# Performance work log

Measured on AMD Instinct MI355X. Metric: run time of the kernel, lower is better.

## Reference

```python
import jax, jax.numpy as jnp
import numpy as np

B, N_OBJ, OBJ_D = 256, 36, 2048
ATT_D, EMB_D, DEC_D, VOCAB, T = 1024, 1024, 1024, 10000, 20


def setup_inputs() -> dict:
    key = jax.random.key(0)
    ks = jax.random.split(key, 16)
    s = lambda *d: 1.0 / np.sqrt(d[-1])
    inp = {
        'encoder_out': jax.random.normal(ks[0], (B, EMB_D), jnp.float32),
        'objects': jax.random.normal(ks[1], (B, N_OBJ, OBJ_D), jnp.float32),
        'encoded_captions': jax.random.randint(ks[2], (B, T), 0, VOCAB),
        'caption_lengths': jax.random.randint(ks[3], (B, 1), 1, T + 1),
        'emb_table': jax.random.normal(ks[4], (VOCAB, EMB_D), jnp.float32) * 0.02,
        'W_enc_att': jax.random.normal(ks[5], (ATT_D, OBJ_D), jnp.float32) * s(OBJ_D),
        'b_enc_att': jnp.zeros((ATT_D,), jnp.float32),
        'W_dec_att': jax.random.normal(ks[6], (ATT_D, DEC_D), jnp.float32) * s(DEC_D),
        'b_dec_att': jnp.zeros((ATT_D,), jnp.float32),
        'w_full_att': jax.random.normal(ks[7], (1, ATT_D), jnp.float32) * s(ATT_D),
        'b_full_att': jnp.zeros((1,), jnp.float32),
        'W_fbeta': jax.random.normal(ks[8], (OBJ_D, DEC_D), jnp.float32) * s(DEC_D),
        'b_fbeta': jnp.zeros((OBJ_D,), jnp.float32),
        'W_ih': jax.random.normal(ks[9], (4 * DEC_D, EMB_D + OBJ_D), jnp.float32) * s(EMB_D + OBJ_D),
        'W_hh': jax.random.normal(ks[10], (4 * DEC_D, DEC_D), jnp.float32) * s(DEC_D),
        'b_ih': jnp.zeros((4 * DEC_D,), jnp.float32),
        'b_hh': jnp.zeros((4 * DEC_D,), jnp.float32),
        'W_fc': jax.random.normal(ks[11], (VOCAB, DEC_D), jnp.float32) * s(DEC_D),
        'b_fc': jnp.zeros((VOCAB,), jnp.float32),
    }
    return inp


def reference(encoder_out, objects, encoded_captions, caption_lengths,
              emb_table, W_enc_att, b_enc_att, W_dec_att, b_dec_att,
              w_full_att, b_full_att, W_fbeta, b_fbeta,
              W_ih, W_hh, b_ih, b_hh, W_fc, b_fc):
    lengths = caption_lengths[:, 0]
    sort_ind = jnp.argsort(-lengths)  # descending
    lengths = lengths[sort_ind]
    encoder_out = encoder_out[sort_ind]
    objects = objects[sort_ind]
    encoded_captions = encoded_captions[sort_ind]

    embeddings = emb_table[encoded_captions]  # (B, T, E)
    # step t input: encoder_out at t=0, embeddings[:, t-1] afterwards
    step_x = jnp.concatenate([encoder_out[:, None, :], embeddings[:, : T - 1, :]], axis=1)  # (B,T,E)

    att1 = jnp.einsum('bno,ao->bna', objects, W_enc_att) + b_enc_att  # (B,N,A), h-independent

    def step(carry, xs):
        h, c = carry
        x_t, t = xs  # (B,E), scalar
        active = (t < lengths)[:, None]  # (B,1) -- batch_size_t masking (lengths sorted desc)
        att2 = h @ W_dec_att.T + b_dec_att  # (B,A)
        e = (jax.nn.relu(att1 + att2[:, None, :]) @ w_full_att[0] + b_full_att[0])  # (B,N)
        alpha = jax.nn.softmax(e, axis=1)
        awe = jnp.einsum('bn,bno->bo', alpha, objects)  # (B,O)
        gate = jax.nn.sigmoid(h @ W_fbeta.T + b_fbeta)
        awe = gate * awe
        gates = jnp.concatenate([x_t, awe], axis=-1) @ W_ih.T + b_ih + h @ W_hh.T + b_hh
        i, f, g, o = jnp.split(gates, 4, axis=-1)  # torch LSTMCell order
        c_new = jax.nn.sigmoid(f) * c + jax.nn.sigmoid(i) * jnp.tanh(g)
        h_new = jax.nn.sigmoid(o) * jnp.tanh(c_new)
        h = jnp.where(active, h_new, h)
        c = jnp.where(active, c_new, c)
        preds = h_new @ W_fc.T + b_fc  # dropout in eval mode = identity
        preds = jnp.where(active, preds, 0.0)
        alpha = jnp.where(active, alpha, 0.0)
        return (h, c), (preds, alpha)

    h0 = jnp.zeros((B, DEC_D), objects.dtype)
    c0 = jnp.zeros((B, DEC_D), objects.dtype)
    xs = (jnp.swapaxes(step_x, 0, 1), jnp.arange(T))
    _, (preds, alphas) = jax.lax.scan(step, (h0, c0), xs)
    predictions = jnp.swapaxes(preds, 0, 1)  # (B,T,V)
    alphas = jnp.swapaxes(alphas, 0, 1)      # (B,T,N)
    return predictions, encoded_captions, lengths, alphas, sort_ind
```

## Files before the change

### kernel.cpp

```cpp
#include <hip/hip_runtime.h>
#include <hip/hip_bf16.h>
#include <cstdint>
#include <cstddef>

#define BB 256
#define TT 20
#define NOBJ 36
#define OBJD 2048
#define ATTD 1024
#define DECD 1024
#define VOCAB 10000
#define NBIG  17168
#define NBIGP 17280
#define NSPLIT 7168

typedef unsigned short u16;
typedef __attribute__((ext_vector_type(8))) short short8v;
typedef __attribute__((ext_vector_type(4))) float float4v;

__device__ inline u16 f2bf(float f) {
    __hip_bfloat16 h = __float2bfloat16(f);
    return *reinterpret_cast<u16*>(&h);
}
__device__ inline float bu(u16 u) {
    union { unsigned int i; float f; } x;
    x.i = ((unsigned int)u) << 16;
    return x.f;
}
__device__ inline float sigf(float x) { return 1.f / (1.f + expf(-x)); }

__device__ inline void gload16(const u16* g, u16* l) {
    __builtin_amdgcn_global_load_lds(
        (const __attribute__((address_space(1))) unsigned int*)g,
        (__attribute__((address_space(3))) unsigned int*)l, 16, 0, 0);
}

__global__ __launch_bounds__(256) void sort_kernel(
    const int* __restrict__ lens, int* __restrict__ sidx, int* __restrict__ slen,
    int* __restrict__ cnt, float* __restrict__ out_len, float* __restrict__ out_sind)
{
    __shared__ int L[BB];
    __shared__ int SL[BB];
    const int i = threadIdx.x;
    const int li = lens[i];
    L[i] = li;
    __syncthreads();
    int r = 0;
    for (int j = 0; j < BB; ++j) {
        const int lj = L[j];
        if (lj > li || (lj == li && j < i)) r++;
    }
    sidx[r] = i;
    slen[r] = li;
    SL[r] = li;
    out_sind[r] = (float)i;
    out_len[r]  = (float)li;
    __syncthreads();
    if (i < TT) {
        int cc = 0;
        for (int b = 0; b < BB; ++b) cc += (SL[b] > i);
        cnt[i] = cc;
    }
}

__global__ __launch_bounds__(256) void meta_kernel(
    const int* __restrict__ caps, const int* __restrict__ sidx,
    float* __restrict__ out_caps)
{
    const int idx = blockIdx.x * 256 + threadIdx.x;
    const int p = idx / TT, t = idx % TT;
    out_caps[idx] = (float)caps[sidx[p] * TT + t];
}

__global__ __launch_bounds__(256) void gather_objs(
    const float* __restrict__ objs, const int* __restrict__ sidx,
    u16* __restrict__ objsb)
{
    const int row = blockIdx.x;
    const int b = row / NOBJ, n = row - b * NOBJ;
    const float* src = objs + ((size_t)sidx[b] * NOBJ + n) * OBJD;
    u16* dst = objsb + (size_t)row * OBJD;
    const int tid = threadIdx.x;
    #pragma unroll
    for (int j = 0; j < 2; ++j) {
        float4 v = ((const float4*)src)[tid + 256 * j];
        ushort4 s;
        s.x = f2bf(v.x); s.y = f2bf(v.y); s.z = f2bf(v.z); s.w = f2bf(v.w);
        ((ushort4*)dst)[tid + 256 * j] = s;
    }
}

__global__ __launch_bounds__(256) void convWbig(
    const float* __restrict__ Wda, const float* __restrict__ bda,
    const float* __restrict__ Wfb, const float* __restrict__ bfb,
    const float* __restrict__ Whh,
    const float* __restrict__ Wfc, const float* __restrict__ bfc,
    u16* __restrict__ Wb, float* __restrict__ bcat)
{
    const int n = blockIdx.x;
    const int tid = threadIdx.x;
    const float* src = nullptr;
    float bb = 0.f;
    if (n < 1024)        { src = Wda + (size_t)n * 1024;            bb = bda[n]; }
    else if (n < 3072)   { src = Wfb + (size_t)(n - 1024) * 1024;   bb = bfb[n - 1024]; }
    else if (n < 7168)   { src = Whh + (size_t)(n - 3072) * 1024;   bb = 0.f; }
    else if (n < NBIG)   { src = Wfc + (size_t)(n - 7168) * 1024;   bb = bfc[n - 7168]; }
    u16* dst = Wb + (size_t)n * 1024;
    ushort4 s;
    if (src) {
        float4 v = ((const float4*)src)[tid];
        s.x = f2bf(v.x); s.y = f2bf(v.y); s.z = f2bf(v.z); s.w = f2bf(v.w);
    } else { s.x = s.y = s.z = s.w = 0; }
    ((ushort4*)dst)[tid] = s;
    if (tid == 0) bcat[n] = bb;
}

__global__ __launch_bounds__(256) void convWih(
    const float* __restrict__ Wih, const float* __restrict__ bih,
    const float* __restrict__ bhh, u16* __restrict__ Wb, float* __restrict__ bsum)
{
    const int n = blockIdx.x;
    const int tid = threadIdx.x;
    const float* src = Wih + (size_t)n * 3072;
    u16* dst = Wb + (size_t)n * 3072;
    #pragma unroll
    for (int j = 0; j < 3; ++j) {
        float4 v = ((const float4*)src)[tid + 256 * j];
        ushort4 s;
        s.x = f2bf(v.x); s.y = f2bf(v.y); s.z = f2bf(v.z); s.w = f2bf(v.w);
        ((ushort4*)dst)[tid + 256 * j] = s;
    }
    if (tid == 0) bsum[n] = bih[n] + bhh[n];
}

__global__ __launch_bounds__(256) void convWea(
    const float* __restrict__ Wea, u16* __restrict__ Wb)
{
    const int n = blockIdx.x;
    const int tid = threadIdx.x;
    const float* src = Wea + (size_t)n * OBJD;
    u16* dst = Wb + (size_t)n * OBJD;
    #pragma unroll
    for (int j = 0; j < 2; ++j) {
        float4 v = ((const float4*)src)[tid + 256 * j];
        ushort4 s;
        s.x = f2bf(v.x); s.y = f2bf(v.y); s.z = f2bf(v.z); s.w = f2bf(v.w);
        ((ushort4*)dst)[tid + 256 * j] = s;
    }
}

__global__ __launch_bounds__(256) void embed_kernel(
    const float* __restrict__ enc, const int* __restrict__ caps,
    const float* __restrict__ emb, const int* __restrict__ sidx,
    u16* __restrict__ Xb)
{
    const int blk = blockIdx.x;
    const int t = blk >> 8;
    const int b = blk & 255;
    const int sb = sidx[b];
    const float* src = (t == 0) ? (enc + (size_t)sb * DECD)
                                : (emb + (size_t)caps[sb * TT + (t - 1)] * DECD);
    const int tid = threadIdx.x;
    float4 v = ((const float4*)src)[tid];
    ushort4 s;
    s.x = f2bf(v.x); s.y = f2bf(v.y); s.z = f2bf(v.z); s.w = f2bf(v.w);
    ((ushort4*)(Xb + (size_t)blk * DECD))[tid] = s;
}

__global__ __launch_bounds__(256) void zero_hc(float* __restrict__ h, float* __restrict__ c)
{
    const int idx = blockIdx.x * 256 + threadIdx.x;
    if (idx < BB * DECD) h[idx] = 0.f;
    else                 c[idx - BB * DECD] = 0.f;
}

__global__ __launch_bounds__(256) void hcat0_kernel(
    const float* __restrict__ bcat, float* __restrict__ Hcat)
{
    const int col4 = blockIdx.x * 256 + threadIdx.x;
    const int m = blockIdx.y;
    ((float4*)(Hcat + (size_t)m * 7168))[col4] = ((const float4*)bcat)[col4];
}

__global__ __launch_bounds__(256) void gemm128(
    const u16* __restrict__ A, int lda,
    const u16* __restrict__ B, int ldb,
    const float* __restrict__ bias,
    float* __restrict__ Cf, u16* __restrict__ Cb, int ldc,
    int Nreal, int kzlen, size_t zCstride, int pairM,
    int nsplit, float* __restrict__ C2, int ldc2, const int* __restrict__ cntp)
{
    __shared__ u16 As[3][128 * 32];
    __shared__ u16 Bs[3][128 * 32];
    const int tid = threadIdx.x;
    const int lane = tid & 63;
    const int w = tid >> 6;
    const int wr = w >> 1, wc = w & 1;
    int nIdx, mIdx;
    if (pairM) { nIdx = blockIdx.x >> 1; mIdx = blockIdx.x & 1; }
    else       { nIdx = blockIdx.x;      mIdx = blockIdx.y; }
    const int m0 = mIdx * 128;
    const int n0 = nIdx * 128;
    const int kbase = blockIdx.z * kzlen;
    A += kbase;
    B += kbase;
    if (Cf) Cf += (size_t)blockIdx.z * zCstride;

    const int act = cntp ? *cntp : (1 << 30);
    float4v acc[4][4];
    #pragma unroll
    for (int i = 0; i < 4; ++i)
        #pragma unroll
        for (int j = 0; j < 4; ++j) acc[i][j] = (float4v){0.f, 0.f, 0.f, 0.f};

    if (m0 < act) {
        const int r0 = (w * 2 + 0) * 16 + (lane >> 2);
        const int r1 = (w * 2 + 1) * 16 + (lane >> 2);
        const int s0 = (lane & 3) ^ ((r0 >> 1) & 3);
        const int s1 = (lane & 3) ^ ((r1 >> 1) & 3);
        const u16* gA0 = A + (size_t)(m0 + r0) * lda + s0 * 8;
        const u16* gA1 = A + (size_t)(m0 + r1) * lda + s1 * 8;
        const u16* gB0 = B + (size_t)(n0 + r0) * ldb + s0 * 8;
        const u16* gB1 = B + (size_t)(n0 + r1) * ldb + s1 * 8;
        const int la0 = (w * 2 + 0) * 16 * 32;
        const int la1 = (w * 2 + 1) * 16 * 32;

        int ia[4], ib[4];
        #pragma unroll
        for (int mi = 0; mi < 4; ++mi) {
            const int r = wr * 64 + mi * 16 + (lane & 15);
            ia[mi] = r * 32 + (((lane >> 4) ^ ((r >> 1) & 3)) << 3);
        }
        #pragma unroll
        for (int nj = 0; nj < 4; ++nj) {
            const int r = wc * 64 + nj * 16 + (lane & 15);
            ib[nj] = r * 32 + (((lane >> 4) ^ ((r >> 1) & 3)) << 3);
        }

        const int nk = kzlen >> 5;
        #pragma unroll
        for (int p = 0; p < 3; ++p) {
            if (p < nk) {
                const int ko = p * 32;
                gload16(gA0 + ko, &As[p][la0]);
                gload16(gA1 + ko, &As[p][la1]);
                gload16(gB0 + ko, &Bs[p][la0]);
                gload16(gB1 + ko, &Bs[p][la1]);
            }
        }
        int cur = 0;
        for (int it = 0; it < nk; ++it) {
            const int rem = nk - 1 - it;
            if (rem >= 2)      asm volatile("s_waitcnt vmcnt(8)" ::: "memory");
            else if (rem == 1) asm volatile("s_waitcnt vmcnt(4)" ::: "memory");
            else               asm volatile("s_waitcnt vmcnt(0)" ::: "memory");
            __builtin_amdgcn_s_barrier();
            short8v av[4], bv[4];
            #pragma unroll
            for (int mi = 0; mi < 4; ++mi) av[mi] = *(const short8v*)&As[cur][ia[mi]];
            #pragma unroll
            for (int nj = 0; nj < 4; ++nj) bv[nj] = *(const short8v*)&Bs[cur][ib[nj]];
            __builtin_amdgcn_s_setprio(1);
            #pragma unroll
            for (int mi = 0; mi < 4; ++mi)
                #pragma unroll
                for (int nj = 0; nj < 4; ++nj)
                    acc[mi][nj] = __builtin_amdgcn_mfma_f32_16x16x32_bf16(
                        av[mi], bv[nj], acc[mi][nj], 0, 0, 0);
            __builtin_amdgcn_s_setprio(0);
            __builtin_amdgcn_s_barrier();
            if (it + 3 < nk) {
                const int ko = (it + 3) * 32;
                gload16(gA0 + ko, &As[cur][la0]);
                gload16(gA1 + ko, &As[cur][la1]);
                gload16(gB0 + ko, &Bs[cur][la0]);
                gload16(gB1 + ko, &Bs[cur][la1]);
            }
            cur = (cur == 2) ? 0 : cur + 1;
        }
    }

    #pragma unroll
    for (int mi = 0; mi < 4; ++mi) {
        const int mbase = m0 + wr * 64 + mi * 16 + ((lane >> 4) << 2);
        #pragma unroll
        for (int nj = 0; nj < 4; ++nj) {
            const int n = n0 + wc * 64 + nj * 16 + (lane & 15);
            if (n >= Nreal) continue;
            const float bval = bias ? bias[n] : 0.f;
            #pragma unroll
            for (int r = 0; r < 4; ++r) {
                const int m = mbase + r;
                const float v = acc[mi][nj][r] + bval;
                if (n < nsplit) {
                    if (Cb) Cb[(size_t)m * ldc + n] = f2bf(v);
                    else    Cf[(size_t)m * ldc + n] = v;
                } else {
                    C2[(size_t)m * ldc2 + (n - nsplit)] = (m < act) ? v : 0.f;
                }
            }
        }
    }
}

__global__ __launch_bounds__(256) void attn_kernel(
    const u16* __restrict__ att1b, const float* __restrict__ Hcat,
    const u16* __restrict__ objsb,
    const float* __restrict__ wfa, const float* __restrict__ bfa,
    const int* __restrict__ slen, int t,
    float* __restrict__ out_alph, u16* __restrict__ aweb)
{
    const int b = blockIdx.x, z = blockIdx.y, tid = threadIdx.x;
    const bool active = t < slen[b];
    if (!active) {
        if (z == 0 && tid < NOBJ)
            out_alph[((size_t)b * TT + t) * NOBJ + tid] = 0.f;
        return;
    }
    __shared__ float wred[4][40];
    __shared__ float es[40];
    __shared__ float alph[40];
    const int lane = tid & 63, w = tid >> 6;
    const float* hrow = Hcat + (size_t)b * 7168;
    const float4 h4 = ((const float4*)hrow)[tid];
    const float4 w4 = ((const float4*)wfa)[tid];
    const u16* a1base = att1b + (size_t)b * NOBJ * ATTD;

    float ep[NOBJ];
    #pragma unroll
    for (int n = 0; n < NOBJ; ++n) {
        ushort4 a4 = ((const ushort4*)(a1base + (size_t)n * ATTD))[tid];
        const float v0 = fmaxf(bu(a4.x) + h4.x, 0.f);
        const float v1 = fmaxf(bu(a4.y) + h4.y, 0.f);
        const float v2 = fmaxf(bu(a4.z) + h4.z, 0.f);
        const float v3 = fmaxf(bu(a4.w) + h4.w, 0.f);
        ep[n] = v0 * w4.x + v1 * w4.y + v2 * w4.z + v3 * w4.w;
    }
    #pragma unroll
    for (int n = 0; n < NOBJ; ++n) {
        float p = ep[n];
        #pragma unroll
        for (int off = 32; off > 0; off >>= 1) p += __shfl_down(p, off, 64);
        if (lane == 0) wred[w][n] = p;
    }
    __syncthreads();
    if (tid < NOBJ)
        es[tid] = wred[0][tid] + wred[1][tid] + wred[2][tid] + wred[3][tid] + bfa[0];
    __syncthreads();
    if (tid < 64) {
        float mv = (tid < NOBJ) ? es[tid] : -1e30f;
        #pragma unroll
        for (int off = 32; off > 0; off >>= 1) mv = fmaxf(mv, __shfl_xor(mv, off, 64));
        float e = (tid < NOBJ) ? expf(es[tid] - mv) : 0.f;
        float s = e;
        #pragma unroll
        for (int off = 32; off > 0; off >>= 1) s += __shfl_xor(s, off, 64);
        if (tid < NOBJ) alph[tid] = e / s;
    }
    __syncthreads();
    if (z == 0 && tid < NOBJ)
        out_alph[((size_t)b * TT + t) * NOBJ + tid] = alph[tid];

    float acc[4] = {0.f, 0.f, 0.f, 0.f};
    const u16* ob = objsb + (size_t)b * NOBJ * OBJD + z * 1024 + tid * 4;
    #pragma unroll 4
    for (int n = 0; n < NOBJ; ++n) {
        const ushort4 ov = *(const ushort4*)(ob + (size_t)n * OBJD);
        const float al = alph[n];
        acc[0] = fmaf(al, bu(ov.x), acc[0]);
        acc[1] = fmaf(al, bu(ov.y), acc[1]);
        acc[2] = fmaf(al, bu(ov.z), acc[2]);
        acc[3] = fmaf(al, bu(ov.w), acc[3]);
    }
    const float4 g0 = *(const float4*)(hrow + 1024 + z * 1024 + tid * 4);
    ushort4 st;
    st.x = f2bf(acc[0] * sigf(g0.x));
    st.y = f2bf(acc[1] * sigf(g0.y));
    st.z = f2bf(acc[2] * sigf(g0.z));
    st.w = f2bf(acc[3] * sigf(g0.w));
    *(ushort4*)&aweb[(size_t)b * 2048 + z * 1024 + tid * 4] = st;
}

__global__ __launch_bounds__(256) void lstm_kernel(
    const float* __restrict__ G2p, const u16* __restrict__ Gxb,
    const float* __restrict__ Hcat,
    float* __restrict__ h, float* __restrict__ c, u16* __restrict__ hb,
    const int* __restrict__ slen, int t)
{
    const int idx = blockIdx.x * 256 + threadIdx.x;
    const int b = idx >> 8, d4 = idx & 255;
    if (t >= slen[b]) return;
    const float4* pw = (const float4*)(Hcat + (size_t)b * 7168 + 3072);
    const u16* gx = Gxb + ((size_t)(t * BB + b)) * 4096;

    float4 g[4];
    #pragma unroll
    for (int q = 0; q < 4; ++q) {
        const ushort4 xv = ((const ushort4*)(gx + q * 1024))[d4];
        float4 s;
        s.x = bu(xv.x); s.y = bu(xv.y); s.z = bu(xv.z); s.w = bu(xv.w);
        const float4 hv = pw[q * 256 + d4];
        s.x += hv.x; s.y += hv.y; s.z += hv.z; s.w += hv.w;
        #pragma unroll
        for (int p = 0; p < 4; ++p) {
            const float4 pv = ((const float4*)G2p)[(size_t)p * (BB * 1024) + b * 1024 + q * 256 + d4];
            s.x += pv.x; s.y += pv.y; s.z += pv.z; s.w += pv.w;
        }
        g[q] = s;
    }
    float4* hp = (float4*)(h + (size_t)b * 1024);
    float4* cp = (float4*)(c + (size_t)b * 1024);
    const float4 cold = cp[d4];
    float4 cn, hn;
    {
        const float si = sigf(g[0].x), sf = sigf(g[1].x), so = sigf(g[3].x);
        cn.x = sf * cold.x + si * tanhf(g[2].x); hn.x = so * tanhf(cn.x);
    }
    {
        const float si = sigf(g[0].y), sf = sigf(g[1].y), so = sigf(g[3].y);
        cn.y = sf * cold.y + si * tanhf(g[2].y); hn.y = so * tanhf(cn.y);
    }
    {
        const float si = sigf(g[0].z), sf = sigf(g[1].z), so = sigf(g[3].z);
        cn.z = sf * cold.z + si * tanhf(g[2].z); hn.z = so * tanhf(cn.z);
    }
    {
        const float si = sigf(g[0].w), sf = sigf(g[1].w), so = sigf(g[3].w);
        cn.w = sf * cold.w + si * tanhf(g[2].w); hn.w = so * tanhf(cn.w);
    }
    hp[d4] = hn;
    cp[d4] = cn;
    ushort4 s;
    s.x = f2bf(hn.x); s.y = f2bf(hn.y); s.z = f2bf(hn.z); s.w = f2bf(hn.w);
    ((ushort4*)(hb + (size_t)b * 1024))[d4] = s;
}

extern "C" void kernel_launch(void* const* d_in, const int* in_sizes, int n_in,
                              void* d_out, int out_size, void* d_ws, size_t ws_size,
                              hipStream_t stream)
{
    const float* enc  = (const float*)d_in[0];
    const float* objs = (const float*)d_in[1];
    const int*   caps = (const int*)d_in[2];
    const int*   clen = (const int*)d_in[3];
    const float* emb  = (const float*)d_in[4];
    const float* Wea  = (const float*)d_in[5];
    const float* bea  = (const float*)d_in[6];
    const float* Wda  = (const float*)d_in[7];
    const float* bda  = (const float*)d_in[8];
    const float* wfa  = (const float*)d_in[9];
    const float* bfa  = (const float*)d_in[10];
    const float* Wfb  = (const float*)d_in[11];
    const float* bfb  = (const float*)d_in[12];
    const float* Wih  = (const float*)d_in[13];
    const float* Whh  = (const float*)d_in[14];
    const float* bih  = (const float*)d_in[15];
    const float* bhh  = (const float*)d_in[16];
    const float* Wfc  = (const float*)d_in[17];
    const float* bfc  = (const float*)d_in[18];

    float* outP     = (float*)d_out;
    float* out_caps = outP + (size_t)BB * TT * VOCAB;
    float* out_len  = out_caps + BB * TT;
    float* out_alph = out_len + BB;
    float* out_sind = out_alph + (size_t)BB * TT * NOBJ;

    char* wp = (char*)d_ws;
    auto alloc = [&](size_t bytes) -> void* {
        void* r = (void*)wp;
        wp += (bytes + 255) & ~(size_t)255;
        return r;
    };
    int*   sidx  = (int*)alloc(BB * 4);
    int*   slen  = (int*)alloc(BB * 4);
    int*   cnt   = (int*)alloc(32 * 4);
    u16*   objsb = (u16*)alloc((size_t)BB * NOBJ * OBJD * 2);
    u16*   Wbigb = (u16*)alloc((size_t)NBIGP * 1024 * 2);
    float* bcat  = (float*)alloc(NBIGP * 4);
    u16*   Wihb  = (u16*)alloc((size_t)4096 * 3072 * 2);
    float* bsum  = (float*)alloc(4096 * 4);
    u16*   Weab  = (u16*)alloc((size_t)1024 * OBJD * 2);
    u16*   att1b = (u16*)alloc((size_t)BB * NOBJ * ATTD * 2);
    u16*   Xb    = (u16*)alloc((size_t)TT * BB * DECD * 2);
    u16*   Gxb   = (u16*)alloc((size_t)TT * BB * 4096 * 2);
    float* Hcat  = (float*)alloc((size_t)BB * 7168 * 4);
    u16*   aweb  = (u16*)alloc((size_t)BB * 2048 * 2);
    float* G2p   = (float*)alloc((size_t)4 * BB * 4096 * 4);
    float* h     = (float*)alloc((size_t)BB * DECD * 4);
    float* c     = (float*)alloc((size_t)BB * DECD * 4);
    u16*   hb    = (u16*)alloc((size_t)BB * DECD * 2);
    (void)ws_size; (void)in_sizes; (void)n_in; (void)out_size;

    sort_kernel<<<1, 256, 0, stream>>>(clen, sidx, slen, cnt, out_len, out_sind);
    meta_kernel<<<20, 256, 0, stream>>>(caps, sidx, out_caps);
    gather_objs<<<BB * NOBJ, 256, 0, stream>>>(objs, sidx, objsb);
    convWbig<<<NBIGP, 256, 0, stream>>>(Wda, bda, Wfb, bfb, Whh, Wfc, bfc, Wbigb, bcat);
    convWih<<<4096, 256, 0, stream>>>(Wih, bih, bhh, Wihb, bsum);
    convWea<<<1024, 256, 0, stream>>>(Wea, Weab);
    embed_kernel<<<TT * BB, 256, 0, stream>>>(enc, caps, emb, sidx, Xb);
    zero_hc<<<2048, 256, 0, stream>>>(h, c);
    hcat0_kernel<<<dim3(7, 256), 256, 0, stream>>>(bcat, Hcat);

    gemm128<<<dim3(8, 72, 1), 256, 0, stream>>>(
        objsb, OBJD, Weab, OBJD, bea, nullptr, att1b, ATTD,
        ATTD, OBJD, 0, 0, 1 << 30, nullptr, 0, nullptr);

    gemm128<<<dim3(32, 40, 1), 256, 0, stream>>>(
        Xb, DECD, Wihb, 3072, bsum, nullptr, Gxb, 4096,
        4096, DECD, 0, 0, 1 << 30, nullptr, 0, nullptr);

    for (int t = 0; t < TT; ++t) {
        attn_kernel<<<dim3(BB, 2), 256, 0, stream>>>(
            att1b, Hcat, objsb, wfa, bfa, slen, t, out_alph, aweb);
        gemm128<<<dim3(64, 1, 4), 256, 0, stream>>>(
            aweb, 2048, Wihb + 1024, 3072, nullptr, G2p, nullptr, 4096,
            4096, 512, (size_t)BB * 4096, 1, 1 << 30, nullptr, 0, cnt + t);
        lstm_kernel<<<256, 256, 0, stream>>>(G2p, Gxb, Hcat, h, c, hb, slen, t);
        gemm128<<<dim3(NBIGP / 64, 1, 1), 256, 0, stream>>>(
            hb, DECD, Wbigb, DECD, bcat, Hcat, nullptr, 7168,
            NBIG, DECD, 0, 1, NSPLIT, outP + (size_t)t * VOCAB, TT * VOCAB, cnt + t);
    }
}
```

Measured before the change: 1.704 ms.

## Fuse LSTM into gate GEMM epilogue and batch vocab projection after recurrence

The W_hh, W_ih and bias rows are reordered so each 128-column tile holds interleaved i/f/g/o gates. This lets a new g2l kernel run the awe-by-W_ih GEMM with full K and apply the LSTM cell update in its epilogue, removing the split-K partials buffer and the separate lstm kernel. The vocabulary projection is taken out of the per-step critical-path GEMM, with every step's h kept in bf16, and run once after the loop as a single large GEMM over all timesteps. The trade-off is that the per-step gate GEMM now uses only 64 blocks with no K split, which gives less parallelism on the serial path.

```diff
diff --git a/kernel.cpp b/kernel.cpp
--- a/kernel.cpp
+++ b/kernel.cpp
@@ -10,13 +10,12 @@
 #define ATTD 1024
 #define DECD 1024
 #define VOCAB 10000
-#define NBIG  17168
-#define NBIGP 17280
-#define NSPLIT 7168
+#define NHC   7168
+#define VOCP  10112
 
 typedef unsigned short u16;
 typedef __attribute__((ext_vector_type(8))) short short8v;
-typedef __attribute__((ext_vector_type(4))) float float4v;
+typedef __attribute__((ext_vector_type(4))) float f32x4;
 
 __device__ inline u16 f2bf(float f) {
     __hip_bfloat16 h = __float2bfloat16(f);
@@ -90,29 +89,40 @@
     }
 }
 
-__global__ __launch_bounds__(256) void convWbig(
+__global__ __launch_bounds__(256) void convWhc(
     const float* __restrict__ Wda, const float* __restrict__ bda,
     const float* __restrict__ Wfb, const float* __restrict__ bfb,
     const float* __restrict__ Whh,
-    const float* __restrict__ Wfc, const float* __restrict__ bfc,
     u16* __restrict__ Wb, float* __restrict__ bcat)
 {
     const int n = blockIdx.x;
     const int tid = threadIdx.x;
-    const float* src = nullptr;
+    const float* src;
     float bb = 0.f;
-    if (n < 1024)        { src = Wda + (size_t)n * 1024;            bb = bda[n]; }
-    else if (n < 3072)   { src = Wfb + (size_t)(n - 1024) * 1024;   bb = bfb[n - 1024]; }
-    else if (n < 7168)   { src = Whh + (size_t)(n - 3072) * 1024;   bb = 0.f; }
-    else if (n < NBIG)   { src = Wfc + (size_t)(n - 7168) * 1024;   bb = bfc[n - 7168]; }
-    u16* dst = Wb + (size_t)n * 1024;
+    if (n < 1024)      { src = Wda + (size_t)n * 1024;          bb = bda[n]; }
+    else if (n < 3072) { src = Wfb + (size_t)(n - 1024) * 1024; bb = bfb[n - 1024]; }
+    else {
+        const int loc = n - 3072, q = loc & 3, d = loc >> 2;
+        src = Whh + ((size_t)q * 1024 + d) * 1024;
+    }
+    float4 v = ((const float4*)src)[tid];
     ushort4 s;
-    if (src) {
-        float4 v = ((const float4*)src)[tid];
+    s.x = f2bf(v.x); s.y = f2bf(v.y); s.z = f2bf(v.z); s.w = f2bf(v.w);
+    ((ushort4*)(Wb + (size_t)n * 1024))[tid] = s;
+    if (tid == 0) bcat[n] = bb;
+}
+
+__global__ __launch_bounds__(256) void convWfc(
+    const float* __restrict__ Wfc, u16* __restrict__ Wb)
+{
+    const int n = blockIdx.x;
+    const int tid = threadIdx.x;
+    ushort4 s;
+    if (n < VOCAB) {
+        float4 v = ((const float4*)(Wfc + (size_t)n * 1024))[tid];
         s.x = f2bf(v.x); s.y = f2bf(v.y); s.z = f2bf(v.z); s.w = f2bf(v.w);
     } else { s.x = s.y = s.z = s.w = 0; }
-    ((ushort4*)dst)[tid] = s;
-    if (tid == 0) bcat[n] = bb;
+    ((ushort4*)(Wb + (size_t)n * 1024))[tid] = s;
 }
 
 __global__ __launch_bounds__(256) void convWih(
@@ -120,8 +130,9 @@
     const float* __restrict__ bhh, u16* __restrict__ Wb, float* __restrict__ bsum)
 {
     const int n = blockIdx.x;
-    const int tid = threadIdx.x;
-    const float* src = Wih + (size_t)n * 3072;
+    const int q = n & 3, d = n >> 2;
+    const int tid = threadIdx.x;
+    const float* src = Wih + ((size_t)q * 1024 + d) * 3072;
     u16* dst = Wb + (size_t)n * 3072;
     #pragma unroll
     for (int j = 0; j < 3; ++j) {
@@ -130,7 +141,7 @@
         s.x = f2bf(v.x); s.y = f2bf(v.y); s.z = f2bf(v.z); s.w = f2bf(v.w);
         ((ushort4*)dst)[tid + 256 * j] = s;
     }
-    if (tid == 0) bsum[n] = bih[n] + bhh[n];
+    if (tid == 0) bsum[n] = bih[q * 1024 + d] + bhh[q * 1024 + d];
 }
 
 __global__ __launch_bounds__(256) void convWea(
@@ -167,11 +178,9 @@
     ((ushort4*)(Xb + (size_t)blk * DECD))[tid] = s;
 }
 
-__global__ __launch_bounds__(256) void zero_hc(float* __restrict__ h, float* __restrict__ c)
-{
-    const int idx = blockIdx.x * 256 + threadIdx.x;
-    if (idx < BB * DECD) h[idx] = 0.f;
-    else                 c[idx - BB * DECD] = 0.f;
+__global__ __launch_bounds__(256) void zero_c(float* __restrict__ c)
+{
+    ((float4*)c)[blockIdx.x * 256 + threadIdx.x] = make_float4(0.f, 0.f, 0.f, 0.f);
 }
 
 __global__ __launch_bounds__(256) void hcat0_kernel(
@@ -179,7 +188,87 @@
 {
     const int col4 = blockIdx.x * 256 + threadIdx.x;
     const int m = blockIdx.y;
-    ((float4*)(Hcat + (size_t)m * 7168))[col4] = ((const float4*)bcat)[col4];
+    ((float4*)(Hcat + (size_t)m * NHC))[col4] = ((const float4*)bcat)[col4];
+}
+
+__device__ __forceinline__ void gemm_core(u16* SH,
+    const u16* __restrict__ A, int lda,
+    const u16* __restrict__ B, int ldb,
+    int K, int m0, int n0, f32x4 acc[4][4])
+{
+    u16* AsB = SH;
+    u16* BsB = SH + 12288;
+    const int tid = threadIdx.x;
+    const int lane = tid & 63;
+    const int w = tid >> 6;
+    const int wr = w >> 1, wc = w & 1;
+
+    const int r0 = (w * 2 + 0) * 16 + (lane >> 2);
+    const int r1 = (w * 2 + 1) * 16 + (lane >> 2);
+    const int s0 = (lane & 3) ^ ((r0 >> 1) & 3);
+    const int s1 = (lane & 3) ^ ((r1 >> 1) & 3);
+    const u16* gA0 = A + (size_t)(m0 + r0) * lda + s0 * 8;
+    const u16* gA1 = A + (size_t)(m0 + r1) * lda + s1 * 8;
+    const u16* gB0 = B + (size_t)(n0 + r0) * ldb + s0 * 8;
+    const u16* gB1 = B + (size_t)(n0 + r1) * ldb + s1 * 8;
+    const int la0 = (w * 2 + 0) * 512;
+    const int la1 = (w * 2 + 1) * 512;
+
+    int ia[4], ib[4];
+    #pragma unroll
+    for (int mi = 0; mi < 4; ++mi) {
+        const int r = wr * 64 + mi * 16 + (lane & 15);
+        ia[mi] = r * 32 + (((lane >> 4) ^ ((r >> 1) & 3)) << 3);
+    }
+    #pragma unroll
+    for (int nj = 0; nj < 4; ++nj) {
+        const int r = wc * 64 + nj * 16 + (lane & 15);
+        ib[nj] = r * 32 + (((lane >> 4) ^ ((r >> 1) & 3)) << 3);
+    }
+
+    const int nk = K >> 5;
+    #pragma unroll
+    for (int p = 0; p < 3; ++p) {
+        if (p < nk) {
+            const int ko = p * 32;
+            gload16(gA0 + ko, AsB + p * 4096 + la0);
+            gload16(gA1 + ko, AsB + p * 4096 + la1);
+            gload16(gB0 + ko, BsB + p * 4096 + la0);
+            gload16(gB1 + ko, BsB + p * 4096 + la1);
+        }
+    }
+    int cur = 0;
+    for (int it = 0; it < nk; ++it) {
+        const int rem = nk - 1 - it;
+        if (rem >= 2)      asm volatile("s_waitcnt vmcnt(8)" ::: "memory");
+        else if (rem == 1) asm volatile("s_waitcnt vmcnt(4)" ::: "memory");
+        else               asm volatile("s_waitcnt vmcnt(0)" ::: "memory");
+        __builtin_amdgcn_s_barrier();
+        const u16* Asc = AsB + cur * 4096;
+        const u16* Bsc = BsB + cur * 4096;
+        short8v av[4], bv[4];
+        #pragma unroll
+        for (int mi = 0; mi < 4; ++mi) av[mi] = *(const short8v*)&Asc[ia[mi]];
+        #pragma unroll
+        for (int nj = 0; nj < 4; ++nj) bv[nj] = *(const short8v*)&Bsc[ib[nj]];
+        __builtin_amdgcn_s_setprio(1);
+        #pragma unroll
+        for (int mi = 0; mi < 4; ++mi)
+            #pragma unroll
+            for (int nj = 0; nj < 4; ++nj)
+                acc[mi][nj] = __builtin_amdgcn_mfma_f32_16x16x32_bf16(
+                    av[mi], bv[nj], acc[mi][nj], 0, 0, 0);
+        __builtin_amdgcn_s_setprio(0);
+        __builtin_amdgcn_s_barrier();
+        if (it + 3 < nk) {
+            const int ko = (it + 3) * 32;
+            gload16(gA0 + ko, AsB + cur * 4096 + la0);
+            gload16(gA1 + ko, AsB + cur * 4096 + la1);
+            gload16(gB0 + ko, BsB + cur * 4096 + la0);
+            gload16(gB1 + ko, BsB + cur * 4096 + la1);
+        }
+        cur = (cur == 2) ? 0 : cur + 1;
+    }
 }
 
 __global__ __launch_bounds__(256) void gemm128(
@@ -187,99 +276,25 @@
     const u16* __restrict__ B, int ldb,
     const float* __restrict__ bias,
     float* __restrict__ Cf, u16* __restrict__ Cb, int ldc,
-    int Nreal, int kzlen, size_t zCstride, int pairM,
-    int nsplit, float* __restrict__ C2, int ldc2, const int* __restrict__ cntp)
-{
-    __shared__ u16 As[3][128 * 32];
-    __shared__ u16 Bs[3][128 * 32];
-    const int tid = threadIdx.x;
-    const int lane = tid & 63;
-    const int w = tid >> 6;
-    const int wr = w >> 1, wc = w & 1;
+    int Nreal, int K, int pairM, const int* __restrict__ cntp)
+{
+    __shared__ __align__(16) u16 SH[24576];
     int nIdx, mIdx;
     if (pairM) { nIdx = blockIdx.x >> 1; mIdx = blockIdx.x & 1; }
     else       { nIdx = blockIdx.x;      mIdx = blockIdx.y; }
     const int m0 = mIdx * 128;
     const int n0 = nIdx * 128;
-    const int kbase = blockIdx.z * kzlen;
-    A += kbase;
-    B += kbase;
-    if (Cf) Cf += (size_t)blockIdx.z * zCstride;
-
-    const int act = cntp ? *cntp : (1 << 30);
-    float4v acc[4][4];
+    if (cntp && m0 >= *cntp) return;
+
+    f32x4 acc[4][4];
     #pragma unroll
     for (int i = 0; i < 4; ++i)
         #pragma unroll
-        for (int j = 0; j < 4; ++j) acc[i][j] = (float4v){0.f, 0.f, 0.f, 0.f};
-
-    if (m0 < act) {
-        const int r0 = (w * 2 + 0) * 16 + (lane >> 2);
-        const int r1 = (w * 2 + 1) * 16 + (lane >> 2);
-        const int s0 = (lane & 3) ^ ((r0 >> 1) & 3);
-        const int s1 = (lane & 3) ^ ((r1 >> 1) & 3);
-        const u16* gA0 = A + (size_t)(m0 + r0) * lda + s0 * 8;
-        const u16* gA1 = A + (size_t)(m0 + r1) * lda + s1 * 8;
-        const u16* gB0 = B + (size_t)(n0 + r0) * ldb + s0 * 8;
-        const u16* gB1 = B + (size_t)(n0 + r1) * ldb + s1 * 8;
-        const int la0 = (w * 2 + 0) * 16 * 32;
-        const int la1 = (w * 2 + 1) * 16 * 32;
-
-        int ia[4], ib[4];
-        #pragma unroll
-        for (int mi = 0; mi < 4; ++mi) {
-            const int r = wr * 64 + mi * 16 + (lane & 15);
-            ia[mi] = r * 32 + (((lane >> 4) ^ ((r >> 1) & 3)) << 3);
-        }
-        #pragma unroll
-        for (int nj = 0; nj < 4; ++nj) {
-            const int r = wc * 64 + nj * 16 + (lane & 15);
-            ib[nj] = r * 32 + (((lane >> 4) ^ ((r >> 1) & 3)) << 3);
-        }
-
-        const int nk = kzlen >> 5;
-        #pragma unroll
-        for (int p = 0; p < 3; ++p) {
-            if (p < nk) {
-                const int ko = p * 32;
-                gload16(gA0 + ko, &As[p][la0]);
-                gload16(gA1 + ko, &As[p][la1]);
-                gload16(gB0 + ko, &Bs[p][la0]);
-                gload16(gB1 + ko, &Bs[p][la1]);
-            }
-        }
-        int cur = 0;
-        for (int it = 0; it < nk; ++it) {
-            const int rem = nk - 1 - it;
-            if (rem >= 2)      asm volatile("s_waitcnt vmcnt(8)" ::: "memory");
-            else if (rem == 1) asm volatile("s_waitcnt vmcnt(4)" ::: "memory");
-            else               asm volatile("s_waitcnt vmcnt(0)" ::: "memory");
-            __builtin_amdgcn_s_barrier();
-            short8v av[4], bv[4];
-            #pragma unroll
-            for (int mi = 0; mi < 4; ++mi) av[mi] = *(const short8v*)&As[cur][ia[mi]];
-            #pragma unroll
-            for (int nj = 0; nj < 4; ++nj) bv[nj] = *(const short8v*)&Bs[cur][ib[nj]];
-            __builtin_amdgcn_s_setprio(1);
-            #pragma unroll
-            for (int mi = 0; mi < 4; ++mi)
-                #pragma unroll
-                for (int nj = 0; nj < 4; ++nj)
-                    acc[mi][nj] = __builtin_amdgcn_mfma_f32_16x16x32_bf16(
-                        av[mi], bv[nj], acc[mi][nj], 0, 0, 0);
-            __builtin_amdgcn_s_setprio(0);
-            __builtin_amdgcn_s_barrier();
-            if (it + 3 < nk) {
-                const int ko = (it + 3) * 32;
-                gload16(gA0 + ko, &As[cur][la0]);
-                gload16(gA1 + ko, &As[cur][la1]);
-                gload16(gB0 + ko, &Bs[cur][la0]);
-                gload16(gB1 + ko, &Bs[cur][la1]);
-            }
-            cur = (cur == 2) ? 0 : cur + 1;
-        }
-    }
-
+        for (int j = 0; j < 4; ++j) acc[i][j] = (f32x4){0.f, 0.f, 0.f, 0.f};
+    gemm_core(SH, A, lda, B, ldb, K, m0, n0, acc);
+
+    const int lane = threadIdx.x & 63, w = threadIdx.x >> 6;
+    const int wr = w >> 1, wc = w & 1;
     #pragma unroll
     for (int mi = 0; mi < 4; ++mi) {
         const int mbase = m0 + wr * 64 + mi * 16 + ((lane >> 4) << 2);
@@ -292,12 +307,110 @@
             for (int r = 0; r < 4; ++r) {
                 const int m = mbase + r;
                 const float v = acc[mi][nj][r] + bval;
-                if (n < nsplit) {
-                    if (Cb) Cb[(size_t)m * ldc + n] = f2bf(v);
-                    else    Cf[(size_t)m * ldc + n] = v;
-                } else {
-                    C2[(size_t)m * ldc2 + (n - nsplit)] = (m < act) ? v : 0.f;
+                if (Cb) Cb[(size_t)m * ldc + n] = f2bf(v);
+                else    Cf[(size_t)m * ldc + n] = v;
+            }
+        }
+    }
+}
+
+__global__ __launch_bounds__(256) void g2l_kernel(
+    const u16* __restrict__ aweb, const u16* __restrict__ Wihb,
+    const u16* __restrict__ Gxb_t, const float* __restrict__ Hcat,
+    float* __restrict__ c, u16* __restrict__ hb_t,
+    const int* __restrict__ cntp)
+{
+    __shared__ __align__(16) u16 SH[24576];
+    const int bid = blockIdx.x, tid = threadIdx.x;
+    const int m0 = (bid & 1) * 128, n0 = (bid >> 1) * 128;
+    const int act = *cntp;
+    if (m0 >= act) return;
+
+    f32x4 acc[4][4];
+    #pragma unroll
+    for (int i = 0; i < 4; ++i)
+        #pragma unroll
+        for (int j = 0; j < 4; ++j) acc[i][j] = (f32x4){0.f, 0.f, 0.f, 0.f};
+    gemm_core(SH, aweb, 2048, Wihb + 1024, 3072, 2048, m0, n0, acc);
+
+    const int lane = tid & 63, w = tid >> 6;
+    const int wr = w >> 1, wc = w & 1;
+    float* patch = (float*)SH;
+    #pragma unroll
+    for (int half = 0; half < 2; ++half) {
+        __syncthreads();
+        if (wr == half) {
+            #pragma unroll
+            for (int mi = 0; mi < 4; ++mi) {
+                const int rbase = mi * 16 + ((lane >> 4) << 2);
+                #pragma unroll
+                for (int nj = 0; nj < 4; ++nj) {
+                    const int col = wc * 64 + nj * 16 + (lane & 15);
+                    #pragma unroll
+                    for (int r = 0; r < 4; ++r)
+                        patch[(rbase + r) * 128 + col] = acc[mi][nj][r];
                 }
+            }
+        }
+        __syncthreads();
+        const int h0 = half * 64;
+        #pragma unroll
+        for (int p8 = 0; p8 < 8; ++p8) {
+            const int idx = p8 * 256 + tid;
+            const int row = idx >> 5, dl = idx & 31;
+            const int b = m0 + h0 + row;
+            if (b >= act) continue;
+            const int d = (n0 >> 2) + dl;
+            const float* pr = patch + row * 128 + dl * 4;
+            float gi = pr[0], gf = pr[1], gg = pr[2], go = pr[3];
+            const ushort4 xv = *(const ushort4*)(Gxb_t + (size_t)b * 4096 + n0 + dl * 4);
+            gi += bu(xv.x); gf += bu(xv.y); gg += bu(xv.z); go += bu(xv.w);
+            const float4 hv = *(const float4*)(Hcat + (size_t)b * NHC + 3072 + n0 + dl * 4);
+            gi += hv.x; gf += hv.y; gg += hv.z; go += hv.w;
+            float* cp = c + (size_t)b * 1024 + d;
+            const float cn = sigf(gf) * cp[0] + sigf(gi) * tanhf(gg);
+            const float hn = sigf(go) * tanhf(cn);
+            cp[0] = cn;
+            hb_t[(size_t)b * 1024 + d] = f2bf(hn);
+        }
+    }
+}
+
+__global__ __launch_bounds__(256) void preds_gemm(
+    const u16* __restrict__ hball, const u16* __restrict__ Wfcb,
+    const float* __restrict__ bfc, const int* __restrict__ cnt,
+    float* __restrict__ outP)
+{
+    __shared__ __align__(16) u16 SH[24576];
+    const int m0 = blockIdx.y * 128;
+    const int n0 = blockIdx.x * 128;
+    const int t = m0 >> 8;
+    const int act = cnt[t];
+    const int bbase = m0 & 255;
+
+    f32x4 acc[4][4];
+    #pragma unroll
+    for (int i = 0; i < 4; ++i)
+        #pragma unroll
+        for (int j = 0; j < 4; ++j) acc[i][j] = (f32x4){0.f, 0.f, 0.f, 0.f};
+    if (bbase < act)
+        gemm_core(SH, hball, 1024, Wfcb, 1024, 1024, m0, n0, acc);
+
+    const int lane = threadIdx.x & 63, w = threadIdx.x >> 6;
+    const int wr = w >> 1, wc = w & 1;
+    #pragma unroll
+    for (int mi = 0; mi < 4; ++mi) {
+        const int mbase = bbase + wr * 64 + mi * 16 + ((lane >> 4) << 2);
+        #pragma unroll
+        for (int nj = 0; nj < 4; ++nj) {
+            const int n = n0 + wc * 64 + nj * 16 + (lane & 15);
+            if (n >= VOCAB) continue;
+            const float bval = bfc[n];
+            #pragma unroll
+            for (int r = 0; r < 4; ++r) {
+                const int b = mbase + r;
+                outP[((size_t)b * TT + t) * VOCAB + n] =
+                    (b < act) ? (acc[mi][nj][r] + bval) : 0.f;
             }
         }
     }
@@ -321,7 +434,7 @@
     __shared__ float es[40];
     __shared__ float alph[40];
     const int lane = tid & 63, w = tid >> 6;
-    const float* hrow = Hcat + (size_t)b * 7168;
+    const float* hrow = Hcat + (size_t)b * NHC;
     const float4 h4 = ((const float4*)hrow)[tid];
     const float4 w4 = ((const float4*)wfa)[tid];
     const u16* a1base = att1b + (size_t)b * NOBJ * ATTD;
@@ -379,60 +492,6 @@
     st.z = f2bf(acc[2] * sigf(g0.z));
     st.w = f2bf(acc[3] * sigf(g0.w));
     *(ushort4*)&aweb[(size_t)b * 2048 + z * 1024 + tid * 4] = st;
-}
-
-__global__ __launch_bounds__(256) void lstm_kernel(
-    const float* __restrict__ G2p, const u16* __restrict__ Gxb,
-    const float* __restrict__ Hcat,
-    float* __restrict__ h, float* __restrict__ c, u16* __restrict__ hb,
-    const int* __restrict__ slen, int t)
-{
-    const int idx = blockIdx.x * 256 + threadIdx.x;
-    const int b = idx >> 8, d4 = idx & 255;
-    if (t >= slen[b]) return;
-    const float4* pw = (const float4*)(Hcat + (size_t)b * 7168 + 3072);
-    const u16* gx = Gxb + ((size_t)(t * BB + b)) * 4096;
-
-    float4 g[4];
-    #pragma unroll
-    for (int q = 0; q < 4; ++q) {
-        const ushort4 xv = ((const ushort4*)(gx + q * 1024))[d4];
-        float4 s;
-        s.x = bu(xv.x); s.y = bu(xv.y); s.z = bu(xv.z); s.w = bu(xv.w);
-        const float4 hv = pw[q * 256 + d4];
-        s.x += hv.x; s.y += hv.y; s.z += hv.z; s.w += hv.w;
-        #pragma unroll
-        for (int p = 0; p < 4; ++p) {
-            const float4 pv = ((const float4*)G2p)[(size_t)p * (BB * 1024) + b * 1024 + q * 256 + d4];
-            s.x += pv.x; s.y += pv.y; s.z += pv.z; s.w += pv.w;
-        }
-        g[q] = s;
-    }
-    float4* hp = (float4*)(h + (size_t)b * 1024);
-    float4* cp = (float4*)(c + (size_t)b * 1024);
-    const float4 cold = cp[d4];
-    float4 cn, hn;
-    {
-        const float si = sigf(g[0].x), sf = sigf(g[1].x), so = sigf(g[3].x);
-        cn.x = sf * cold.x + si * tanhf(g[2].x); hn.x = so * tanhf(cn.x);
-    }
-    {
-        const float si = sigf(g[0].y), sf = sigf(g[1].y), so = sigf(g[3].y);
-        cn.y = sf * cold.y + si * tanhf(g[2].y); hn.y = so * tanhf(cn.y);
-    }
-    {
-        const float si = sigf(g[0].z), sf = sigf(g[1].z), so = sigf(g[3].z);
-        cn.z = sf * cold.z + si * tanhf(g[2].z); hn.z = so * tanhf(cn.z);
-    }
-    {
-        const float si = sigf(g[0].w), sf = sigf(g[1].w), so = sigf(g[3].w);
-        cn.w = sf * cold.w + si * tanhf(g[2].w); hn.w = so * tanhf(cn.w);
-    }
-    hp[d4] = hn;
-    cp[d4] = cn;
-    ushort4 s;
-    s.x = f2bf(hn.x); s.y = f2bf(hn.y); s.z = f2bf(hn.z); s.w = f2bf(hn.w);
-    ((ushort4*)(hb + (size_t)b * 1024))[d4] = s;
 }
 
 extern "C" void kernel_launch(void* const* d_in, const int* in_sizes, int n_in,
@@ -475,49 +534,52 @@
     int*   slen  = (int*)alloc(BB * 4);
     int*   cnt   = (int*)alloc(32 * 4);
     u16*   objsb = (u16*)alloc((size_t)BB * NOBJ * OBJD * 2);
-    u16*   Wbigb = (u16*)alloc((size_t)NBIGP * 1024 * 2);
-    float* bcat  = (float*)alloc(NBIGP * 4);
+    u16*   Whcb  = (u16*)alloc((size_t)NHC * 1024 * 2);
+    float* bcat  = (float*)alloc(NHC * 4);
+    u16*   Wfcb  = (u16*)alloc((size_t)VOCP * 1024 * 2);
     u16*   Wihb  = (u16*)alloc((size_t)4096 * 3072 * 2);
     float* bsum  = (float*)alloc(4096 * 4);
     u16*   Weab  = (u16*)alloc((size_t)1024 * OBJD * 2);
     u16*   att1b = (u16*)alloc((size_t)BB * NOBJ * ATTD * 2);
     u16*   Xb    = (u16*)alloc((size_t)TT * BB * DECD * 2);
     u16*   Gxb   = (u16*)alloc((size_t)TT * BB * 4096 * 2);
-    float* Hcat  = (float*)alloc((size_t)BB * 7168 * 4);
+    float* Hcat  = (float*)alloc((size_t)BB * NHC * 4);
     u16*   aweb  = (u16*)alloc((size_t)BB * 2048 * 2);
-    float* G2p   = (float*)alloc((size_t)4 * BB * 4096 * 4);
-    float* h     = (float*)alloc((size_t)BB * DECD * 4);
+    u16*   hball = (u16*)alloc((size_t)TT * BB * DECD * 2);
     float* c     = (float*)alloc((size_t)BB * DECD * 4);
-    u16*   hb    = (u16*)alloc((size_t)BB * DECD * 2);
     (void)ws_size; (void)in_sizes; (void)n_in; (void)out_size;
 
     sort_kernel<<<1, 256, 0, stream>>>(clen, sidx, slen, cnt, out_len, out_sind);
     meta_kernel<<<20, 256, 0, stream>>>(caps, sidx, out_caps);
     gather_objs<<<BB * NOBJ, 256, 0, stream>>>(objs, sidx, objsb);
-    convWbig<<<NBIGP, 256, 0, stream>>>(Wda, bda, Wfb, bfb, Whh, Wfc, bfc, Wbigb, bcat);
+    convWhc<<<NHC, 256, 0, stream>>>(Wda, bda, Wfb, bfb, Whh, Whcb, bcat);
+    convWfc<<<VOCP, 256, 0, stream>>>(Wfc, Wfcb);
     convWih<<<4096, 256, 0, stream>>>(Wih, bih, bhh, Wihb, bsum);
     convWea<<<1024, 256, 0, stream>>>(Wea, Weab);
     embed_kernel<<<TT * BB, 256, 0, stream>>>(enc, caps, emb, sidx, Xb);
-    zero_hc<<<2048, 256, 0, stream>>>(h, c);
+    zero_c<<<256, 256, 0, stream>>>(c);
     hcat0_kernel<<<dim3(7, 256), 256, 0, stream>>>(bcat, Hcat);
 
-    gemm128<<<dim3(8, 72, 1), 256, 0, stream>>>(
+    gemm128<<<dim3(8, 72), 256, 0, stream>>>(
         objsb, OBJD, Weab, OBJD, bea, nullptr, att1b, ATTD,
-        ATTD, OBJD, 0, 0, 1 << 30, nullptr, 0, nullptr);
-
-    gemm128<<<dim3(32, 40, 1), 256, 0, stream>>>(
+        ATTD, OBJD, 0, nullptr);
+
+    gemm128<<<dim3(32, 40), 256, 0, stream>>>(
         Xb, DECD, Wihb, 3072, bsum, nullptr, Gxb, 4096,
-        4096, DECD, 0, 0, 1 << 30, nullptr, 0, nullptr);
+        4096, DECD, 0, nullptr);
 
     for (int t = 0; t < TT; ++t) {
         attn_kernel<<<dim3(BB, 2), 256, 0, stream>>>(
             att1b, Hcat, objsb, wfa, bfa, slen, t, out_alph, aweb);
-        gemm128<<<dim3(64, 1, 4), 256, 0, stream>>>(
-            aweb, 2048, Wihb + 1024, 3072, nullptr, G2p, nullptr, 4096,
-            4096, 512, (size_t)BB * 4096, 1, 1 << 30, nullptr, 0, cnt + t);
-        lstm_kernel<<<256, 256, 0, stream>>>(G2p, Gxb, Hcat, h, c, hb, slen, t);
-        gemm128<<<dim3(NBIGP / 64, 1, 1), 256, 0, stream>>>(
-            hb, DECD, Wbigb, DECD, bcat, Hcat, nullptr, 7168,
-            NBIG, DECD, 0, 1, NSPLIT, outP + (size_t)t * VOCAB, TT * VOCAB, cnt + t);
-    }
-}
+        g2l_kernel<<<64, 256, 0, stream>>>(
+            aweb, Wihb, Gxb + (size_t)t * BB * 4096, Hcat, c,
+            hball + (size_t)t * BB * DECD, cnt + t);
+        if (t < TT - 1)
+            gemm128<<<112, 256, 0, stream>>>(
+                hball + (size_t)t * BB * DECD, DECD, Whcb, DECD, bcat,
+                Hcat, nullptr, NHC, NHC, DECD, 1, cnt + t);
+    }
+
+    preds_gemm<<<dim3(VOCP / 128, 40), 256, 0, stream>>>(
+        hball, Wfcb, bfc, cnt, outP);
+}
```

Measured after the change: 1.728 ms. Within noise of the previous version (+1.4%).
